# Kernel optimization log

Measured on AMD Instinct MI355X. Metric: run time of the kernel, lower is better.

The kernel has to match this reference:

```python
import jax, jax.numpy as jnp
import numpy as np

CODE_DIM = 256
HIDDEN = 128
HEADS = 4
N_CODES = 100000
N_SPEC = 256


def setup_inputs() -> dict:
    key = jax.random.key(0)
    ks = jax.random.split(key, 7)
    provider_emb = jax.random.normal(ks[0], (CODE_DIM,), jnp.float32)
    code_embs = jax.random.normal(ks[1], (N_CODES, CODE_DIM), jnp.float32)
    # per-head Linear(code_dim -> hidden): stacked weights [H, D, K] and bias [H, K]
    W = jax.random.normal(ks[2], (HEADS, CODE_DIM, HIDDEN), jnp.float32) / np.sqrt(CODE_DIM)
    b = jax.random.normal(ks[3], (HEADS, HIDDEN), jnp.float32) * 0.01
    # attention vectors a: [H, 2*hidden] (squeezed trailing 1)
    a = jax.random.normal(ks[4], (HEADS, 2 * HIDDEN), jnp.float32) * 0.01
    # classifier Linear(hidden*heads -> num_specialties)
    Wc = jax.random.normal(ks[5], (N_SPEC, HIDDEN * HEADS), jnp.float32) / np.sqrt(HIDDEN * HEADS)
    bc = jax.random.normal(ks[6], (N_SPEC,), jnp.float32) * 0.01
    return {"provider_emb": provider_emb, "code_embs": code_embs,
            "W": W, "b": b, "a": a, "Wc": Wc, "bc": bc}


def reference(provider_emb, code_embs, W, b, a, Wc, bc):
    # provider projection per head: [H, K]
    provider_h = jnp.einsum('d,hdk->hk', provider_emb, W) + b
    # code projection per head: [H, N, K]
    code_h = jnp.einsum('nd,hdk->hnk', code_embs, W) + b[:, None, :]
    a1, a2 = a[:, :HIDDEN], a[:, HIDDEN:]           # split concat attention vec
    # e[h,n] = leaky_relu(provider_h[h].a1[h] + code_h[h,n].a2[h])
    e = jnp.einsum('hk,hk->h', provider_h, a1)[:, None] \
        + jnp.einsum('hnk,hk->hn', code_h, a2)
    e = jnp.where(e >= 0, e, 0.2 * e)               # LeakyReLU(0.2)
    alpha = jax.nn.softmax(e, axis=1)               # softmax over code nodes
    # dropout is identity in eval mode
    agg = jnp.einsum('hn,hnk->hk', alpha, code_h)   # weighted sum per head
    multi_head_output = agg.reshape(-1)             # [H*K]
    specialty_logits = multi_head_output @ Wc.T + bc
    return specialty_logits, multi_head_output
```

## Files before the change

kernel.cpp:

```cpp
#include <hip/hip_runtime.h>
#include <hip/hip_bf16.h>

#define CODE_DIM 256
#define HIDDEN   128
#define HEADS    4
#define N_CODES  100000
#define N_SPEC   256

#define K2_BLOCKS 782
#define K2_TPB    256
#define K2_WPB    4
#define K2_AWAVES 3125
#define WROWS     8
#define NTILES    (N_CODES / WROWS)
#define NSLOTS    64

#define WS_V       0
#define WS_CP      1024
#define WS_SLOT    1104
#define SLOT_STRIDE 1028

#define WAITCNT_LGKM0 0xC07F

__global__ void k1_prep(const float* __restrict__ pe, const float* __restrict__ W,
                        const float* __restrict__ b, const float* __restrict__ a,
                        float* __restrict__ ws) {
    const int bx = blockIdx.x;
    const int h = bx >> 4, dseg = bx & 15;
    const int tid = threadIdx.x;
    const int dl = tid >> 4;
    const int q  = tid & 15;
    const int d  = dseg * 16 + dl;
    __shared__ float a_sh[2 * HIDDEN];
    __shared__ float cred[4];
    a_sh[tid] = a[h * 2 * HIDDEN + tid];
    __syncthreads();

    const float4* wr = (const float4*)(W + ((size_t)(h * CODE_DIM + d)) * HIDDEN + q * 8);
    float u = 0.f, v = 0.f;
#pragma unroll
    for (int j = 0; j < 2; ++j) {
        float4 wv = wr[j];
        int k = q * 8 + j * 4;
        u += wv.x * a_sh[k]     + wv.y * a_sh[k + 1]
           + wv.z * a_sh[k + 2] + wv.w * a_sh[k + 3];
        v += wv.x * a_sh[HIDDEN + k]     + wv.y * a_sh[HIDDEN + k + 1]
           + wv.z * a_sh[HIDDEN + k + 2] + wv.w * a_sh[HIDDEN + k + 3];
    }
#pragma unroll
    for (int off = 1; off < 16; off <<= 1) {
        u += __shfl_xor(u, off, 64);
        v += __shfl_xor(v, off, 64);
    }
    if (q == 0) ws[WS_V + h * CODE_DIM + d] = v;

    float cp = (q == 0) ? pe[d] * u : 0.f;
    if (dseg == 0 && tid < HIDDEN) cp += b[h * HIDDEN + tid] * (a_sh[tid] + a_sh[HIDDEN + tid]);
#pragma unroll
    for (int off = 32; off; off >>= 1) cp += __shfl_xor(cp, off, 64);
    if ((tid & 63) == 0) cred[tid >> 6] = cp;
    __syncthreads();
    if (tid == 0) ws[WS_CP + bx] = cred[0] + cred[1] + cred[2] + cred[3];

    float4* z = (float4*)(ws + WS_SLOT);
    const int g = bx * 256 + tid;
    const int nz = (NSLOTS * SLOT_STRIDE) / 4;
    z[g] = make_float4(0.f, 0.f, 0.f, 0.f);
    if (g + 16384 < nz) z[g + 16384] = make_float4(0.f, 0.f, 0.f, 0.f);
}

__global__ __launch_bounds__(K2_TPB, 4) void k2_main(const float* __restrict__ code,
                                                     float* __restrict__ ws) {
    __shared__ float t_sh[K2_WPB * 32];
    __shared__ float eps[K2_WPB * HEADS * CODE_DIM];
    __shared__ float dsh[K2_WPB * HEADS];
    __shared__ float c_sh[HEADS];
    const int tid  = threadIdx.x;
    const int lane = tid & 63;
    const int w    = tid >> 6;
    const int bx   = blockIdx.x;
    const int wid  = bx * K2_WPB + w;

    if (tid < 64) {
        float cpv = ws[WS_CP + tid];
#pragma unroll
        for (int off = 1; off < 16; off <<= 1) cpv += __shfl_xor(cpv, off, 64);
        if ((tid & 15) == 0) c_sh[tid >> 4] = cpv;
    }
    float4 vh[HEADS];
#pragma unroll
    for (int h = 0; h < HEADS; ++h)
        vh[h] = ((const float4*)(ws + WS_V + h * CODE_DIM))[lane];
    __syncthreads();
    const float cme = c_sh[lane & 3];

    float4 acc0 = make_float4(0,0,0,0), acc1 = acc0, acc2 = acc0, acc3 = acc0;
    float dloc = 0.f;

    for (int tile = wid; tile < NTILES; tile += K2_AWAVES) {
        const float4* rp = (const float4*)(code + (size_t)tile * (WROWS * CODE_DIM));
        float4 x[WROWS];
#pragma unroll
        for (int r = 0; r < WROWS; ++r) x[r] = rp[r * 64 + lane];

        float p[32];
#pragma unroll
        for (int r = 0; r < WROWS; ++r) {
            p[r * 4 + 0] = x[r].x * vh[0].x + x[r].y * vh[0].y + x[r].z * vh[0].z + x[r].w * vh[0].w;
            p[r * 4 + 1] = x[r].x * vh[1].x + x[r].y * vh[1].y + x[r].z * vh[1].z + x[r].w * vh[1].w;
            p[r * 4 + 2] = x[r].x * vh[2].x + x[r].y * vh[2].y + x[r].z * vh[2].z + x[r].w * vh[2].w;
            p[r * 4 + 3] = x[r].x * vh[3].x + x[r].y * vh[3].y + x[r].z * vh[3].z + x[r].w * vh[3].w;
        }
#pragma unroll
        for (int k = 0; k < 5; ++k) {
            const int m = 1 << k;
            const bool hi = (lane & m) != 0;
            const int nv = 16 >> k;
#pragma unroll
            for (int i = 0; i < nv; ++i) {
                float keep = hi ? p[2 * i + 1] : p[2 * i];
                float send = hi ? p[2 * i]     : p[2 * i + 1];
                p[i] = keep + __shfl_xor(send, m, 64);
            }
        }
        float tot = p[0] + __shfl_xor(p[0], 32, 64);

        float e = tot + cme;
        e = (e >= 0.f) ? e : 0.2f * e;
        float t = __expf(e);
        dloc += t;

        if (lane < 32) t_sh[w * 32 + lane] = t;
        __builtin_amdgcn_s_waitcnt(WAITCNT_LGKM0);

#pragma unroll
        for (int r = 0; r < WROWS; ++r) {
            float4 tr = *(const float4*)&t_sh[w * 32 + r * 4];
            acc0.x += tr.x * x[r].x; acc0.y += tr.x * x[r].y; acc0.z += tr.x * x[r].z; acc0.w += tr.x * x[r].w;
            acc1.x += tr.y * x[r].x; acc1.y += tr.y * x[r].y; acc1.z += tr.y * x[r].z; acc1.w += tr.y * x[r].w;
            acc2.x += tr.z * x[r].x; acc2.y += tr.z * x[r].y; acc2.z += tr.z * x[r].z; acc2.w += tr.z * x[r].w;
            acc3.x += tr.w * x[r].x; acc3.y += tr.w * x[r].y; acc3.z += tr.w * x[r].z; acc3.w += tr.w * x[r].w;
        }
    }

#pragma unroll
    for (int off = 4; off < 64; off <<= 1) dloc += __shfl_xor(dloc, off, 64);
    if (lane < HEADS) dsh[w * HEADS + lane] = dloc * 0.5f;

    *(float4*)&eps[w * 1024 +   0 + 4 * lane] = acc0;
    *(float4*)&eps[w * 1024 + 256 + 4 * lane] = acc1;
    *(float4*)&eps[w * 1024 + 512 + 4 * lane] = acc2;
    *(float4*)&eps[w * 1024 + 768 + 4 * lane] = acc3;
    __syncthreads();

    float* slot = ws + WS_SLOT + (size_t)(bx & (NSLOTS - 1)) * SLOT_STRIDE;
    for (int o = tid; o < HEADS * CODE_DIM; o += K2_TPB) {
        float s = eps[o] + eps[1024 + o] + eps[2048 + o] + eps[3072 + o];
        atomicAdd(slot + o, s);
    }
    if (tid < HEADS)
        atomicAdd(slot + HEADS * CODE_DIM + tid,
                  dsh[tid] + dsh[4 + tid] + dsh[8 + tid] + dsh[12 + tid]);
}

__global__ void k3_agg(const float* __restrict__ W, const float* __restrict__ b,
                       const float* __restrict__ ws, float* __restrict__ out) {
    const int bx = blockIdx.x;
    const int h = bx >> 2, q = bx & 3;
    const int tid = threadIdx.x;
    __shared__ float s_sh[CODE_DIM];
    __shared__ float yred[8 * 32];
    __shared__ float den_sh;
    const float* slots = ws + WS_SLOT;

    if (tid < 64) {
        float dv = slots[(size_t)tid * SLOT_STRIDE + HEADS * CODE_DIM + h];
#pragma unroll
        for (int off = 32; off; off >>= 1) dv += __shfl_xor(dv, off, 64);
        if (tid == 0) den_sh = dv;
    }
    float su = 0.f;
#pragma unroll 8
    for (int s2 = 0; s2 < NSLOTS; ++s2)
        su += slots[(size_t)s2 * SLOT_STRIDE + h * CODE_DIM + tid];
    __syncthreads();
    s_sh[tid] = su / den_sh;
    __syncthreads();

    const int c = tid >> 5, kl = tid & 31;
    float y = 0.f;
    const float* wp = W + ((size_t)(h * CODE_DIM + c * 32)) * HIDDEN + q * 32 + kl;
#pragma unroll 8
    for (int d = 0; d < 32; ++d) y += s_sh[c * 32 + d] * wp[(size_t)d * HIDDEN];
    yred[c * 32 + kl] = y;
    __syncthreads();
    if (tid < 32) {
        float t = 0.f;
#pragma unroll
        for (int cc = 0; cc < 8; ++cc) t += yred[cc * 32 + tid];
        out[N_SPEC + h * HIDDEN + q * 32 + tid] = t + b[h * HIDDEN + q * 32 + tid];
    }
}

__global__ void k4_logits(const float* __restrict__ Wc, const float* __restrict__ bc,
                          float* __restrict__ out) {
    const int lane = threadIdx.x & 63;
    const int wv   = threadIdx.x >> 6;
    const int i    = blockIdx.x * 4 + wv;
    const float4* wr  = (const float4*)(Wc + (size_t)i * (HEADS * HIDDEN));
    const float4* mh4 = (const float4*)(out + N_SPEC);
    float4 wa = wr[lane],      ma = mh4[lane];
    float4 wb = wr[64 + lane], mb = mh4[64 + lane];
    float pp = wa.x * ma.x + wa.y * ma.y + wa.z * ma.z + wa.w * ma.w
             + wb.x * mb.x + wb.y * mb.y + wb.z * mb.z + wb.w * mb.w;
#pragma unroll
    for (int off = 32; off; off >>= 1) pp += __shfl_xor(pp, off, 64);
    if (lane == 0) out[i] = pp + bc[i];
}

extern "C" void kernel_launch(void* const* d_in, const int* in_sizes, int n_in,
                              void* d_out, int out_size, void* d_ws, size_t ws_size,
                              hipStream_t stream) {
    const float* pe   = (const float*)d_in[0];
    const float* code = (const float*)d_in[1];
    const float* W    = (const float*)d_in[2];
    const float* b    = (const float*)d_in[3];
    const float* a    = (const float*)d_in[4];
    const float* Wc   = (const float*)d_in[5];
    const float* bc   = (const float*)d_in[6];
    float* out = (float*)d_out;
    float* ws  = (float*)d_ws;

    k1_prep<<<64, 256, 0, stream>>>(pe, W, b, a, ws);
    k2_main<<<K2_BLOCKS, K2_TPB, 0, stream>>>(code, ws);
    k3_agg<<<16, 256, 0, stream>>>(W, b, ws, out);
    k4_logits<<<64, 256, 0, stream>>>(Wc, bc, out);
}
```

Before: 178.7 us.

## Double-buffer code tile loads in main kernel and reduce block count

The main streaming loop now prefetches the next tile of code rows into a second register buffer while the current tile is processed, so global-load latency overlaps with compute. The butterfly reduction's first stage is folded into the per-row dot product, which cuts the live partial-sum array from 32 to 16 registers. Block count drops to 768 and launch bounds to 3 blocks per CU to make room for the extra registers, at the cost of lower occupancy and a slightly uneven tile distribution.

```diff
diff --git a/kernel.cpp b/kernel.cpp
--- a/kernel.cpp
+++ b/kernel.cpp
@@ -7,10 +7,10 @@
 #define N_CODES  100000
 #define N_SPEC   256
 
-#define K2_BLOCKS 782
+#define K2_BLOCKS 768
 #define K2_TPB    256
 #define K2_WPB    4
-#define K2_AWAVES 3125
+#define K2_WAVES  (K2_BLOCKS * K2_WPB)
 #define WROWS     8
 #define NTILES    (N_CODES / WROWS)
 #define NSLOTS    64
@@ -69,7 +69,7 @@
     if (g + 16384 < nz) z[g + 16384] = make_float4(0.f, 0.f, 0.f, 0.f);
 }
 
-__global__ __launch_bounds__(K2_TPB, 4) void k2_main(const float* __restrict__ code,
+__global__ __launch_bounds__(K2_TPB, 3) void k2_main(const float* __restrict__ code,
                                                      float* __restrict__ ws) {
     __shared__ float t_sh[K2_WPB * 32];
     __shared__ float eps[K2_WPB * HEADS * CODE_DIM];
@@ -97,22 +97,30 @@
     float4 acc0 = make_float4(0,0,0,0), acc1 = acc0, acc2 = acc0, acc3 = acc0;
     float dloc = 0.f;
 
-    for (int tile = wid; tile < NTILES; tile += K2_AWAVES) {
-        const float4* rp = (const float4*)(code + (size_t)tile * (WROWS * CODE_DIM));
-        float4 x[WROWS];
-#pragma unroll
-        for (int r = 0; r < WROWS; ++r) x[r] = rp[r * 64 + lane];
-
-        float p[32];
+    float4 xA[WROWS], xB[WROWS];
+
+    auto prefetch = [&](float4* xr, int t) {
+        const float4* rp = (const float4*)(code + (size_t)t * (WROWS * CODE_DIM));
+#pragma unroll
+        for (int r = 0; r < WROWS; ++r) xr[r] = rp[r * 64 + lane];
+    };
+
+    auto process = [&](const float4* x) {
+        float p[16];
+        const bool hi0 = (lane & 1) != 0;
 #pragma unroll
         for (int r = 0; r < WROWS; ++r) {
-            p[r * 4 + 0] = x[r].x * vh[0].x + x[r].y * vh[0].y + x[r].z * vh[0].z + x[r].w * vh[0].w;
-            p[r * 4 + 1] = x[r].x * vh[1].x + x[r].y * vh[1].y + x[r].z * vh[1].z + x[r].w * vh[1].w;
-            p[r * 4 + 2] = x[r].x * vh[2].x + x[r].y * vh[2].y + x[r].z * vh[2].z + x[r].w * vh[2].w;
-            p[r * 4 + 3] = x[r].x * vh[3].x + x[r].y * vh[3].y + x[r].z * vh[3].z + x[r].w * vh[3].w;
+            float q0 = x[r].x * vh[0].x + x[r].y * vh[0].y + x[r].z * vh[0].z + x[r].w * vh[0].w;
+            float q1 = x[r].x * vh[1].x + x[r].y * vh[1].y + x[r].z * vh[1].z + x[r].w * vh[1].w;
+            float q2 = x[r].x * vh[2].x + x[r].y * vh[2].y + x[r].z * vh[2].z + x[r].w * vh[2].w;
+            float q3 = x[r].x * vh[3].x + x[r].y * vh[3].y + x[r].z * vh[3].z + x[r].w * vh[3].w;
+            float k0 = hi0 ? q1 : q0, s0 = hi0 ? q0 : q1;
+            float k1 = hi0 ? q3 : q2, s1 = hi0 ? q2 : q3;
+            p[2 * r]     = k0 + __shfl_xor(s0, 1, 64);
+            p[2 * r + 1] = k1 + __shfl_xor(s1, 1, 64);
         }
 #pragma unroll
-        for (int k = 0; k < 5; ++k) {
+        for (int k = 1; k < 5; ++k) {
             const int m = 1 << k;
             const bool hi = (lane & m) != 0;
             const int nv = 16 >> k;
@@ -141,6 +149,20 @@
             acc2.x += tr.z * x[r].x; acc2.y += tr.z * x[r].y; acc2.z += tr.z * x[r].z; acc2.w += tr.z * x[r].w;
             acc3.x += tr.w * x[r].x; acc3.y += tr.w * x[r].y; acc3.z += tr.w * x[r].z; acc3.w += tr.w * x[r].w;
         }
+    };
+
+    int t = wid;
+    prefetch(xA, t);
+    while (true) {
+        int tn = t + K2_WAVES;
+        if (tn < NTILES) prefetch(xB, tn);
+        process(xA);
+        if (tn >= NTILES) break;
+        int tm = tn + K2_WAVES;
+        if (tm < NTILES) prefetch(xA, tm);
+        process(xB);
+        if (tm >= NTILES) break;
+        t = tm;
     }
 
 #pragma unroll
```

Result: no change. 178.4 us (-0.1%).
